# Kernel tuning notes

Measured on AMD Instinct MI355X. Metric: run time of the kernel, lower is better.

## Reference

```python
import jax, jax.numpy as jnp
import numpy as np

TEMPERATURE = 22.627417  # ~sqrt(512)


def setup_inputs() -> dict:
    key = jax.random.key(0)
    ks = jax.random.split(key, 7)
    B, NP, NQ, D = 4, 256, 256, 512
    return {
        "q": jax.random.normal(ks[0], (B, NP, D), jnp.float32),
        "k": jax.random.normal(ks[1], (B, NP, D), jnp.float32),
        "v": jax.random.normal(ks[2], (B, NP, D), jnp.float32),
        "query": jax.random.normal(ks[3], (B, NQ, D), jnp.float32),
        "query_q": jax.random.normal(ks[4], (B, NQ, D), jnp.float32),
        "query_k": jax.random.normal(ks[5], (B, NP, D), jnp.float32),
        "query_v": jax.random.normal(ks[6], (B, NQ, D), jnp.float32),
    }


def reference(q, k, v, query, query_q, query_k, query_v):
    # Self-attention block over prototypes: [B, NP, NP]
    scores = jnp.einsum("bpd,bqd->bpq", q, k) / TEMPERATURE
    log_attn = jax.nn.log_softmax(scores, axis=2)
    attn = jax.nn.softmax(scores, axis=2)
    # NOTE: torch.bmm(attn, v) in the original is dead code (overwritten), so it is skipped.

    # Query-gated attention: [B, NQ, NP]
    q_scores = jnp.einsum("bnd,bpd->bnp", query_q, query_k) / TEMPERATURE
    query_attn = jax.nn.softmax(q_scores, axis=2)

    # Gated broadcast combine: [B, NQ, NP, D]
    # query_attn * v_rep + query_attn * query_v == query_attn * (v + query_v)
    gate = query_attn[:, :, :, None]            # [B, NQ, NP, 1]
    combined = v[:, None, :, :] + query_v[:, :, None, :]  # [B, NQ, NP, D]
    output = gate * combined
    return (output, attn, log_attn)
```

## Files before the change

kernel.cpp:

```cpp
#include <hip/hip_runtime.h>
#include <math.h>

#define BB   4
#define NP   256
#define NQ   256
#define DD   512
#define DD4  (DD / 4)

typedef float f32x4 __attribute__((ext_vector_type(4)));

static constexpr float kScale = 1.0f / 22.627417f;

__global__ __launch_bounds__(256) void scores_softmax4_kernel(
    const float* __restrict__ qmat,
    const float* __restrict__ kmat,
    float* __restrict__ attn_out,
    float* __restrict__ logattn_out)
{
    const int b  = blockIdx.y;
    const int p0 = blockIdx.x * 4;
    const int t  = threadIdx.x;

    const f32x4* krow = (const f32x4*)(kmat + ((size_t)b * 256 + t) * DD);
    const float* qb   = qmat + ((size_t)b * NP + p0) * DD;

    float acc[4] = {0.f, 0.f, 0.f, 0.f};
    #pragma unroll 8
    for (int d4 = 0; d4 < DD4; ++d4) {
        const f32x4 kv = krow[d4];
        #pragma unroll
        for (int r = 0; r < 4; ++r) {
            const float* qr = qb + r * DD + d4 * 4;
            acc[r] += qr[0] * kv.x + qr[1] * kv.y + qr[2] * kv.z + qr[3] * kv.w;
        }
    }

    __shared__ __align__(16) float ss[4][256];
    #pragma unroll
    for (int r = 0; r < 4; ++r) ss[r][t] = acc[r] * kScale;
    __syncthreads();

    const int r = t >> 6;
    const int g = t & 63;
    const f32x4 sv = ((const f32x4*)ss[r])[g];

    float m = fmaxf(fmaxf(sv.x, sv.y), fmaxf(sv.z, sv.w));
    #pragma unroll
    for (int off = 32; off >= 1; off >>= 1) m = fmaxf(m, __shfl_xor(m, off, 64));

    f32x4 ev;
    ev.x = expf(sv.x - m); ev.y = expf(sv.y - m);
    ev.z = expf(sv.z - m); ev.w = expf(sv.w - m);
    float s = ev.x + ev.y + ev.z + ev.w;
    #pragma unroll
    for (int off = 32; off >= 1; off >>= 1) s += __shfl_xor(s, off, 64);

    const float inv = 1.0f / s;
    const float lse = logf(s);

    const size_t base = ((size_t)b * NP + (p0 + r)) * 256;
    ((f32x4*)(attn_out + base))[g] = ev * inv;
    if (logattn_out != nullptr) {
        f32x4 lg;
        lg.x = (sv.x - m) - lse; lg.y = (sv.y - m) - lse;
        lg.z = (sv.z - m) - lse; lg.w = (sv.w - m) - lse;
        ((f32x4*)(logattn_out + base))[g] = lg;
    }
}

__global__ __launch_bounds__(256) void gate_combine2_kernel(
    const float* __restrict__ gate,
    const f32x4* __restrict__ v4,
    const f32x4* __restrict__ qv4,
    f32x4* __restrict__ out4)
{
    const int bn = blockIdx.x;
    const int b  = bn >> 8;
    const int n  = bn & (NQ - 1);
    const int t  = threadIdx.x;
    const int d4 = t & (DD4 - 1);
    const int po = t >> 7;

    const f32x4 qvr = qv4[((size_t)b * NQ + n) * DD4 + d4];
    const float* grow = gate + ((size_t)b * NQ + n) * NP;
    const f32x4* vcol = v4 + (size_t)b * NP * DD4 + d4;
    f32x4* ocol = out4 + ((size_t)b * NQ + n) * ((size_t)NP * DD4) + d4;

    #pragma unroll 4
    for (int p = po; p < NP; p += 2) {
        const float gpn = grow[p];
        const f32x4 vv  = vcol[(size_t)p * DD4];
        const f32x4 o   = (vv + qvr) * gpn;
        __builtin_nontemporal_store(o, ocol + (size_t)p * DD4);
    }
}

extern "C" void kernel_launch(void* const* d_in, const int* in_sizes, int n_in,
                              void* d_out, int out_size, void* d_ws, size_t ws_size,
                              hipStream_t stream) {
    const float* q  = (const float*)d_in[0];
    const float* k  = (const float*)d_in[1];
    const float* v  = (const float*)d_in[2];
    const float* qq = (const float*)d_in[4];
    const float* qk = (const float*)d_in[5];
    const float* qv = (const float*)d_in[6];

    float* out = (float*)d_out;
    const size_t out_elems = (size_t)BB * NQ * NP * DD;
    float* attn_out    = out + out_elems;
    float* logattn_out = attn_out + (size_t)BB * NP * 256;

    dim3 sgrid(NP / 4, BB);

    scores_softmax4_kernel<<<sgrid, 256, 0, stream>>>(qq, qk, attn_out, nullptr);

    gate_combine2_kernel<<<BB * NQ, 256, 0, stream>>>(
        attn_out, (const f32x4*)v, (const f32x4*)qv, (f32x4*)out);

    scores_softmax4_kernel<<<sgrid, 256, 0, stream>>>(q, k, attn_out, logattn_out);
}
```

Measured before the change: 151.8 us.

## Fuse query-score softmax, gated combine and self-attention into one launch

Replaces three kernel launches with a single kernel. Each of the first B*NQ blocks computes its own query-attention row (dot products, softmax) and keeps it in shared memory to gate the broadcast combine. The remaining blocks compute the self-attention softmax and log-softmax. This removes the launch gaps and the global round trip of the gate matrix. The cost is that each block now computes one score row with 256 threads each reading a full qk row, so the dot-product work loses the previous 4-row reuse of qk.

```diff
diff --git a/kernel.cpp b/kernel.cpp
--- a/kernel.cpp
+++ b/kernel.cpp
@@ -11,87 +11,121 @@
 
 static constexpr float kScale = 1.0f / 22.627417f;
 
-__global__ __launch_bounds__(256) void scores_softmax4_kernel(
-    const float* __restrict__ qmat,
-    const float* __restrict__ kmat,
+__global__ __launch_bounds__(256) void fused_qgsa_kernel(
+    const float* __restrict__ q,
+    const float* __restrict__ k,
+    const f32x4* __restrict__ v4,
+    const float* __restrict__ qq,
+    const float* __restrict__ qk,
+    const f32x4* __restrict__ qv4,
+    f32x4* __restrict__ out4,
     float* __restrict__ attn_out,
     float* __restrict__ logattn_out)
 {
-    const int b  = blockIdx.y;
-    const int p0 = blockIdx.x * 4;
-    const int t  = threadIdx.x;
+    __shared__ __align__(16) float smem[4 * 256];
+    __shared__ float red[8];
+    const int t = threadIdx.x;
 
-    const f32x4* krow = (const f32x4*)(kmat + ((size_t)b * 256 + t) * DD);
-    const float* qb   = qmat + ((size_t)b * NP + p0) * DD;
+    if (blockIdx.x < (unsigned)(BB * NQ)) {
+        const int bn = blockIdx.x;
+        const int b  = bn >> 8;
+        const int n  = bn & (NQ - 1);
+        const int w  = t >> 6;
+        const int l  = t & 63;
 
-    float acc[4] = {0.f, 0.f, 0.f, 0.f};
-    #pragma unroll 8
-    for (int d4 = 0; d4 < DD4; ++d4) {
-        const f32x4 kv = krow[d4];
+        float val;
+        {
+            const f32x4* krow = (const f32x4*)(qk + ((size_t)b * NP + t) * DD);
+            const float* qrow = qq + ((size_t)b * NQ + n) * DD;
+            float acc = 0.f;
+            #pragma unroll 8
+            for (int d4 = 0; d4 < DD4; ++d4) {
+                const f32x4 kv = krow[d4];
+                const float* qr = qrow + d4 * 4;
+                acc += qr[0] * kv.x + qr[1] * kv.y + qr[2] * kv.z + qr[3] * kv.w;
+            }
+            val = acc * kScale;
+        }
+
+        float m = val;
         #pragma unroll
-        for (int r = 0; r < 4; ++r) {
-            const float* qr = qb + r * DD + d4 * 4;
-            acc[r] += qr[0] * kv.x + qr[1] * kv.y + qr[2] * kv.z + qr[3] * kv.w;
+        for (int off = 32; off >= 1; off >>= 1) m = fmaxf(m, __shfl_xor(m, off, 64));
+        if (l == 0) red[w] = m;
+        __syncthreads();
+        m = fmaxf(fmaxf(red[0], red[1]), fmaxf(red[2], red[3]));
+
+        const float e = expf(val - m);
+        float s = e;
+        #pragma unroll
+        for (int off = 32; off >= 1; off >>= 1) s += __shfl_xor(s, off, 64);
+        if (l == 0) red[4 + w] = s;
+        __syncthreads();
+        s = (red[4] + red[5]) + (red[6] + red[7]);
+
+        smem[t] = e / s;
+        __syncthreads();
+
+        const int d4 = t & (DD4 - 1);
+        const int po = t >> 7;
+        const f32x4 qvr = qv4[((size_t)b * NQ + n) * DD4 + d4];
+        const f32x4* vcol = v4 + (size_t)b * NP * DD4 + d4;
+        f32x4* ocol = out4 + ((size_t)b * NQ + n) * ((size_t)NP * DD4) + d4;
+
+        #pragma unroll 4
+        for (int p = po; p < NP; p += 2) {
+            const float gpn = smem[p];
+            const f32x4 vv  = vcol[(size_t)p * DD4];
+            const f32x4 o   = (vv + qvr) * gpn;
+            __builtin_nontemporal_store(o, ocol + (size_t)p * DD4);
         }
-    }
+    } else {
+        const int idx = blockIdx.x - BB * NQ;
+        const int b   = idx >> 6;
+        const int p0  = (idx & 63) * 4;
 
-    __shared__ __align__(16) float ss[4][256];
-    #pragma unroll
-    for (int r = 0; r < 4; ++r) ss[r][t] = acc[r] * kScale;
-    __syncthreads();
+        const f32x4* krow = (const f32x4*)(k + ((size_t)b * NP + t) * DD);
+        const float* qb   = q + ((size_t)b * NP + p0) * DD;
 
-    const int r = t >> 6;
-    const int g = t & 63;
-    const f32x4 sv = ((const f32x4*)ss[r])[g];
+        float acc[4] = {0.f, 0.f, 0.f, 0.f};
+        #pragma unroll 8
+        for (int d4 = 0; d4 < DD4; ++d4) {
+            const f32x4 kv = krow[d4];
+            #pragma unroll
+            for (int r = 0; r < 4; ++r) {
+                const float* qr = qb + r * DD + d4 * 4;
+                acc[r] += qr[0] * kv.x + qr[1] * kv.y + qr[2] * kv.z + qr[3] * kv.w;
+            }
+        }
 
-    float m = fmaxf(fmaxf(sv.x, sv.y), fmaxf(sv.z, sv.w));
-    #pragma unroll
-    for (int off = 32; off >= 1; off >>= 1) m = fmaxf(m, __shfl_xor(m, off, 64));
+        float (*ss)[256] = (float (*)[256])smem;
+        #pragma unroll
+        for (int r = 0; r < 4; ++r) ss[r][t] = acc[r] * kScale;
+        __syncthreads();
 
-    f32x4 ev;
-    ev.x = expf(sv.x - m); ev.y = expf(sv.y - m);
-    ev.z = expf(sv.z - m); ev.w = expf(sv.w - m);
-    float s = ev.x + ev.y + ev.z + ev.w;
-    #pragma unroll
-    for (int off = 32; off >= 1; off >>= 1) s += __shfl_xor(s, off, 64);
+        const int r = t >> 6;
+        const int g = t & 63;
+        const f32x4 sv = ((const f32x4*)ss[r])[g];
 
-    const float inv = 1.0f / s;
-    const float lse = logf(s);
+        float m = fmaxf(fmaxf(sv.x, sv.y), fmaxf(sv.z, sv.w));
+        #pragma unroll
+        for (int off = 32; off >= 1; off >>= 1) m = fmaxf(m, __shfl_xor(m, off, 64));
 
-    const size_t base = ((size_t)b * NP + (p0 + r)) * 256;
-    ((f32x4*)(attn_out + base))[g] = ev * inv;
-    if (logattn_out != nullptr) {
+        f32x4 ev;
+        ev.x = expf(sv.x - m); ev.y = expf(sv.y - m);
+        ev.z = expf(sv.z - m); ev.w = expf(sv.w - m);
+        float s = (ev.x + ev.y) + (ev.z + ev.w);
+        #pragma unroll
+        for (int off = 32; off >= 1; off >>= 1) s += __shfl_xor(s, off, 64);
+
+        const float inv = 1.0f / s;
+        const float lse = logf(s);
+
+        const size_t base = ((size_t)b * NP + (p0 + r)) * 256;
+        ((f32x4*)(attn_out + base))[g] = ev * inv;
         f32x4 lg;
         lg.x = (sv.x - m) - lse; lg.y = (sv.y - m) - lse;
         lg.z = (sv.z - m) - lse; lg.w = (sv.w - m) - lse;
         ((f32x4*)(logattn_out + base))[g] = lg;
-    }
-}
-
-__global__ __launch_bounds__(256) void gate_combine2_kernel(
-    const float* __restrict__ gate,
-    const f32x4* __restrict__ v4,
-    const f32x4* __restrict__ qv4,
-    f32x4* __restrict__ out4)
-{
-    const int bn = blockIdx.x;
-    const int b  = bn >> 8;
-    const int n  = bn & (NQ - 1);
-    const int t  = threadIdx.x;
-    const int d4 = t & (DD4 - 1);
-    const int po = t >> 7;
-
-    const f32x4 qvr = qv4[((size_t)b * NQ + n) * DD4 + d4];
-    const float* grow = gate + ((size_t)b * NQ + n) * NP;
-    const f32x4* vcol = v4 + (size_t)b * NP * DD4 + d4;
-    f32x4* ocol = out4 + ((size_t)b * NQ + n) * ((size_t)NP * DD4) + d4;
-
-    #pragma unroll 4
-    for (int p = po; p < NP; p += 2) {
-        const float gpn = grow[p];
-        const f32x4 vv  = vcol[(size_t)p * DD4];
-        const f32x4 o   = (vv + qvr) * gpn;
-        __builtin_nontemporal_store(o, ocol + (size_t)p * DD4);
     }
 }
 
@@ -110,12 +144,7 @@
     float* attn_out    = out + out_elems;
     float* logattn_out = attn_out + (size_t)BB * NP * 256;
 
-    dim3 sgrid(NP / 4, BB);
-
-    scores_softmax4_kernel<<<sgrid, 256, 0, stream>>>(qq, qk, attn_out, nullptr);
-
-    gate_combine2_kernel<<<BB * NQ, 256, 0, stream>>>(
-        attn_out, (const f32x4*)v, (const f32x4*)qv, (f32x4*)out);
-
-    scores_softmax4_kernel<<<sgrid, 256, 0, stream>>>(q, k, attn_out, logattn_out);
+    fused_qgsa_kernel<<<BB * NQ + 256, 256, 0, stream>>>(
+        q, k, (const f32x4*)v, qq, qk, (const f32x4*)qv,
+        (f32x4*)out, attn_out, logattn_out);
 }
```

Result: faster. 131.9 us (-13.1%).
